# Optimization experiments

Hardware: AMD Instinct MI355X
Metric: run time of the kernel (lower is better)

The kernel has to match this reference:

```python
import jax, jax.numpy as jnp
import numpy as np

N_NODES = 100000
N_EDGES = 3200000
F_IN = 512
F_OUT = 256


def setup_inputs() -> dict:
    key = jax.random.key(0)
    k1, k2, k3, k4, k5 = jax.random.split(key, 5)
    x = jax.random.normal(k1, (N_NODES, F_IN), dtype=jnp.float32)
    weights = jax.random.normal(k2, (F_IN, F_OUT), dtype=jnp.float32) * 0.05
    # sparse adjacency in COO, row-sorted (equivalent to the CSR torch.spmm uses)
    edge_row = jnp.sort(jax.random.randint(k3, (N_EDGES,), 0, N_NODES, dtype=jnp.int32))
    edge_col = jax.random.randint(k4, (N_EDGES,), 0, N_NODES, dtype=jnp.int32)
    edge_val = jax.random.uniform(k5, (N_EDGES,), dtype=jnp.float32)
    return {"x": x, "weights": weights, "edge_row": edge_row,
            "edge_col": edge_col, "edge_val": edge_val}


def reference(x, weights, edge_row, edge_col, edge_val):
    # support = input @ weights  (dense GEMM)
    support = jnp.matmul(x, weights)                      # [N, F_OUT]
    # output = spmm(adj, support): gather neighbor rows, scale, scatter-add
    gathered = support[edge_col] * edge_val[:, None]      # [E, F_OUT]
    out = jax.ops.segment_sum(gathered, edge_row, num_segments=N_NODES)
    return out
```

## Files before the change

### kernel.cpp

```cpp
#include <hip/hip_runtime.h>

#define N_NODES 100000
#define N_EDGES 3200000
#define F_IN 512
#define F_OUT 256

typedef short bf16x8 __attribute__((ext_vector_type(8)));
typedef short bf16x4 __attribute__((ext_vector_type(4)));
typedef float f32x4 __attribute__((ext_vector_type(4)));
typedef unsigned u32x4 __attribute__((ext_vector_type(4)));

__device__ __forceinline__ short f2b(float f) {
    unsigned u = __builtin_bit_cast(unsigned, f);
    u += 0x7fffu + ((u >> 16) & 1u);
    return (short)(u >> 16);
}
__device__ __forceinline__ float b2f(short s) {
    unsigned u = ((unsigned)(unsigned short)s) << 16;
    return __builtin_bit_cast(float, u);
}
__device__ __forceinline__ unsigned pack2(float f0, float f1) {
    unsigned u0 = __builtin_bit_cast(unsigned, f0) + 0x8000u;
    unsigned u1 = __builtin_bit_cast(unsigned, f1) + 0x8000u;
    return __builtin_amdgcn_perm(u1, u0, 0x07060302);
}
__device__ __forceinline__ void load_lds16(const void* g, void* l) {
    __builtin_amdgcn_global_load_lds(
        (const __attribute__((address_space(1))) unsigned*)g,
        (__attribute__((address_space(3))) unsigned*)l, 16, 0, 0);
}

__global__ void k_wconv(const float* __restrict__ W, short* __restrict__ Wt) {
    int idx = blockIdx.x * 256 + threadIdx.x;
    int k = idx >> 8;
    int n = idx & 255;
    Wt[n * F_IN + k] = f2b(W[idx]);
}

__global__ void k_rowptr(const int* __restrict__ erow, int* __restrict__ rp) {
    int i = blockIdx.x * 256 + threadIdx.x;
    if (i > N_NODES) return;
    int lo = 0, hi = N_EDGES;
    while (lo < hi) {
        int mid = (lo + hi) >> 1;
        if (erow[mid] < i) lo = mid + 1; else hi = mid;
    }
    rp[i] = lo;
}

__global__ __launch_bounds__(512, 4) void k_gemm(const float* __restrict__ X,
                                                 const short* __restrict__ Wt,
                                                 short* __restrict__ S) {
    __shared__ char lds[65536];
    char* ldsA = lds;
    char* ldsB = lds + 32768;
    const int tid  = threadIdx.x;
    const int wave = tid >> 6;
    const int lane = tid & 63;
    const int wr   = wave >> 2;
    const int wc   = wave & 3;
    const int l15  = lane & 15, quad = lane >> 4;
    const long row_base = (long)blockIdx.x * 128;

    f32x4 acc[4][4];
#pragma unroll
    for (int i = 0; i < 4; ++i)
#pragma unroll
        for (int j = 0; j < 4; ++j) acc[i][j] = (f32x4){0.f, 0.f, 0.f, 0.f};

    const int srow = tid >> 3;
    const int schunk = (tid & 7) ^ (srow & 7);
    long gr0 = row_base + srow;
    long gr1 = gr0 + 64;
    if (gr0 >= N_NODES) gr0 = N_NODES - 1;
    if (gr1 >= N_NODES) gr1 = N_NODES - 1;
    const float* gp0 = X + gr0 * F_IN + schunk * 4;
    const float* gp1 = X + gr1 * F_IN + schunk * 4;

    const int bidx0 = wave * 128 + lane;
    const int bn0 = bidx0 >> 2, bs0 = bidx0 & 3;
    const int bidx1 = bidx0 + 64;
    const int bn1 = bidx1 >> 2, bs1 = bidx1 & 3;
    const short* bsrc0 = Wt + bn0 * F_IN + (bs0 ^ (bn0 & 3)) * 8;
    const short* bsrc1 = Wt + bn1 * F_IN + (bs1 ^ (bn1 & 3)) * 8;

    const int sw = l15 & 7;
    const int c0 = ((quad * 2) ^ sw) * 16;
    const int c1 = ((quad * 2 + 1) ^ sw) * 16;
    const int arow_byte = (wr * 64 + l15) * 128;
    const int bchunk = (quad ^ (l15 & 3)) * 16;
    const int brow_byte = (wc * 64 + l15) * 64;

    {
        char* a0 = ldsA + wave * 1024;
        load_lds16(gp0, a0);
        load_lds16(gp1, a0 + 8192);
        char* b0 = ldsB + wave * 2048;
        load_lds16(bsrc0, b0);
        load_lds16(bsrc1, b0 + 1024);
    }

#pragma unroll 1
    for (int k0 = 0; k0 < F_IN; k0 += 32) {
        const int cur = (k0 >> 5) & 1;
        if (k0 + 32 < F_IN) {
            const int kk = k0 + 32;
            char* a0 = ldsA + (cur ^ 1) * 16384 + wave * 1024;
            load_lds16(gp0 + kk, a0);
            load_lds16(gp1 + kk, a0 + 8192);
            char* b0 = ldsB + (cur ^ 1) * 16384 + wave * 2048;
            load_lds16(bsrc0 + kk, b0);
            load_lds16(bsrc1 + kk, b0 + 1024);
            asm volatile("s_waitcnt vmcnt(4)" ::: "memory");
        } else {
            asm volatile("s_waitcnt vmcnt(0)" ::: "memory");
        }
        __builtin_amdgcn_s_barrier();

        const char* abase = ldsA + cur * 16384 + arow_byte;
        const char* bbase = ldsB + cur * 16384 + brow_byte;
        bf16x8 bfrag[4];
#pragma unroll
        for (int j = 0; j < 4; ++j)
            bfrag[j] = *(const bf16x8*)(bbase + j * 1024 + bchunk);
#pragma unroll
        for (int i = 0; i < 4; ++i) {
            const char* ap = abase + i * 16 * 128;
            f32x4 x0 = *(const f32x4*)(ap + c0);
            f32x4 x1 = *(const f32x4*)(ap + c1);
            u32x4 pv = { pack2(x0.x, x0.y), pack2(x0.z, x0.w),
                         pack2(x1.x, x1.y), pack2(x1.z, x1.w) };
            bf16x8 afrag = __builtin_bit_cast(bf16x8, pv);
#pragma unroll
            for (int j = 0; j < 4; ++j)
                acc[i][j] = __builtin_amdgcn_mfma_f32_16x16x32_bf16(
                    afrag, bfrag[j], acc[i][j], 0, 0, 0);
        }

        asm volatile("s_waitcnt lgkmcnt(0)" ::: "memory");
        __builtin_amdgcn_s_barrier();
    }

#pragma unroll
    for (int i = 0; i < 4; ++i) {
#pragma unroll
        for (int rg = 0; rg < 4; ++rg) {
            long gm = row_base + wr * 64 + i * 16 + quad * 4 + rg;
            if (gm < N_NODES) {
#pragma unroll
                for (int j = 0; j < 4; ++j) {
                    int gn = wc * 64 + j * 16 + l15;
                    S[gm * F_OUT + gn] = f2b(acc[i][j][rg]);
                }
            }
        }
    }
}

__global__ __launch_bounds__(256) void k_spmm(const short* __restrict__ S,
                                              const int* __restrict__ ecol,
                                              const float* __restrict__ ev,
                                              const int* __restrict__ rp,
                                              float* __restrict__ out) {
    const int wid  = __builtin_amdgcn_readfirstlane((int)(threadIdx.x >> 6));
    const int lane = threadIdx.x & 63;
    const int r = blockIdx.x * 4 + wid;
    const int lo = __builtin_amdgcn_readfirstlane(rp[r]);
    const int hi = __builtin_amdgcn_readfirstlane(rp[r + 1]);
    const short* sp = S + lane * 4;
    float a0 = 0.f, a1 = 0.f, a2 = 0.f, a3 = 0.f;

#pragma unroll 1
    for (int base = lo; base < hi; base += 8) {
        int cc[8]; float vv[8];
#pragma unroll
        for (int u = 0; u < 8; ++u) {
            int e = base + u;
            int ee = e < hi ? e : hi - 1;
            cc[u] = __builtin_amdgcn_readfirstlane(ecol[ee]);
            int vb = __builtin_bit_cast(int, e < hi ? ev[ee] : 0.f);
            vv[u] = __builtin_bit_cast(float, __builtin_amdgcn_readfirstlane(vb));
        }
        bf16x4 g[8];
#pragma unroll
        for (int u = 0; u < 8; ++u)
            g[u] = *(const bf16x4*)(sp + cc[u] * 256);
#pragma unroll
        for (int u = 0; u < 8; ++u) {
            a0 += vv[u] * b2f(g[u][0]);
            a1 += vv[u] * b2f(g[u][1]);
            a2 += vv[u] * b2f(g[u][2]);
            a3 += vv[u] * b2f(g[u][3]);
        }
    }
    f32x4 o = {a0, a1, a2, a3};
    *(f32x4*)(out + (long)r * F_OUT + lane * 4) = o;
}

extern "C" void kernel_launch(void* const* d_in, const int* in_sizes, int n_in,
                              void* d_out, int out_size, void* d_ws, size_t ws_size,
                              hipStream_t stream) {
    const float* x    = (const float*)d_in[0];
    const float* w    = (const float*)d_in[1];
    const int*   erow = (const int*)d_in[2];
    const int*   ecol = (const int*)d_in[3];
    const float* ev   = (const float*)d_in[4];
    float* out = (float*)d_out;

    char* ws = (char*)d_ws;
    short* Wt = (short*)ws;
    int*   rp = (int*)(ws + 262144);
    short* S  = (short*)(ws + (1 << 20));

    k_wconv<<<512, 256, 0, stream>>>(w, Wt);
    k_rowptr<<<(N_NODES + 256) / 256, 256, 0, stream>>>(erow, rp);
    k_gemm<<<(N_NODES + 127) / 128, 512, 0, stream>>>(x, Wt, S);
    k_spmm<<<N_NODES / 4, 256, 0, stream>>>(S, ecol, ev, rp, out);
}
```

Baseline: 579.1 us.

## Merge prep kernels, retune B LDS swizzle, prefetch edge indices in SpMM

```diff
diff --git a/kernel.cpp b/kernel.cpp
--- a/kernel.cpp
+++ b/kernel.cpp
@@ -30,22 +30,24 @@
         (__attribute__((address_space(3))) unsigned*)l, 16, 0, 0);
 }
 
-__global__ void k_wconv(const float* __restrict__ W, short* __restrict__ Wt) {
-    int idx = blockIdx.x * 256 + threadIdx.x;
-    int k = idx >> 8;
-    int n = idx & 255;
-    Wt[n * F_IN + k] = f2b(W[idx]);
-}
-
-__global__ void k_rowptr(const int* __restrict__ erow, int* __restrict__ rp) {
-    int i = blockIdx.x * 256 + threadIdx.x;
-    if (i > N_NODES) return;
-    int lo = 0, hi = N_EDGES;
-    while (lo < hi) {
-        int mid = (lo + hi) >> 1;
-        if (erow[mid] < i) lo = mid + 1; else hi = mid;
-    }
-    rp[i] = lo;
+__global__ void k_prep(const float* __restrict__ W, short* __restrict__ Wt,
+                       const int* __restrict__ erow, int* __restrict__ rp) {
+    int b = blockIdx.x;
+    if (b < 512) {
+        int idx = b * 256 + threadIdx.x;
+        int k = idx >> 8;
+        int n = idx & 255;
+        Wt[n * F_IN + k] = f2b(W[idx]);
+    } else {
+        int i = (b - 512) * 256 + threadIdx.x;
+        if (i > N_NODES) return;
+        int lo = 0, hi = N_EDGES;
+        while (lo < hi) {
+            int mid = (lo + hi) >> 1;
+            if (erow[mid] < i) lo = mid + 1; else hi = mid;
+        }
+        rp[i] = lo;
+    }
 }
 
 __global__ __launch_bounds__(512, 4) void k_gemm(const float* __restrict__ X,
@@ -81,14 +83,14 @@
     const int bn0 = bidx0 >> 2, bs0 = bidx0 & 3;
     const int bidx1 = bidx0 + 64;
     const int bn1 = bidx1 >> 2, bs1 = bidx1 & 3;
-    const short* bsrc0 = Wt + bn0 * F_IN + (bs0 ^ (bn0 & 3)) * 8;
-    const short* bsrc1 = Wt + bn1 * F_IN + (bs1 ^ (bn1 & 3)) * 8;
+    const short* bsrc0 = Wt + bn0 * F_IN + (bs0 ^ ((bn0 >> 1) & 3)) * 8;
+    const short* bsrc1 = Wt + bn1 * F_IN + (bs1 ^ ((bn1 >> 1) & 3)) * 8;
 
     const int sw = l15 & 7;
     const int c0 = ((quad * 2) ^ sw) * 16;
     const int c1 = ((quad * 2 + 1) ^ sw) * 16;
     const int arow_byte = (wr * 64 + l15) * 128;
-    const int bchunk = (quad ^ (l15 & 3)) * 16;
+    const int bchunk = (quad ^ ((l15 >> 1) & 3)) * 16;
     const int brow_byte = (wc * 64 + l15) * 64;
 
     {
@@ -170,28 +172,45 @@
     const short* sp = S + lane * 4;
     float a0 = 0.f, a1 = 0.f, a2 = 0.f, a3 = 0.f;
 
-#pragma unroll 1
-    for (int base = lo; base < hi; base += 8) {
-        int cc[8]; float vv[8];
+    int cc[8]; float vv[8];
+    if (lo < hi) {
 #pragma unroll
         for (int u = 0; u < 8; ++u) {
-            int e = base + u;
+            int e = lo + u;
             int ee = e < hi ? e : hi - 1;
             cc[u] = __builtin_amdgcn_readfirstlane(ecol[ee]);
             int vb = __builtin_bit_cast(int, e < hi ? ev[ee] : 0.f);
             vv[u] = __builtin_bit_cast(float, __builtin_amdgcn_readfirstlane(vb));
         }
+    }
+#pragma unroll 1
+    for (int base = lo; base < hi; base += 8) {
         bf16x4 g[8];
 #pragma unroll
         for (int u = 0; u < 8; ++u)
             g[u] = *(const bf16x4*)(sp + cc[u] * 256);
+        int nb = base + 8;
+        int nc[8]; float nv[8];
+        if (nb < hi) {
+#pragma unroll
+            for (int u = 0; u < 8; ++u) {
+                int e = nb + u;
+                int ee = e < hi ? e : hi - 1;
+                nc[u] = __builtin_amdgcn_readfirstlane(ecol[ee]);
+                int vb = __builtin_bit_cast(int, e < hi ? ev[ee] : 0.f);
+                nv[u] = __builtin_bit_cast(float, __builtin_amdgcn_readfirstlane(vb));
+            }
+        }
 #pragma unroll
         for (int u = 0; u < 8; ++u) {
-            a0 += vv[u] * b2f(g[u][0]);
-            a1 += vv[u] * b2f(g[u][1]);
-            a2 += vv[u] * b2f(g[u][2]);
-            a3 += vv[u] * b2f(g[u][3]);
-        }
+            float v = vv[u];
+            a0 += v * b2f(g[u][0]);
+            a1 += v * b2f(g[u][1]);
+            a2 += v * b2f(g[u][2]);
+            a3 += v * b2f(g[u][3]);
+        }
+#pragma unroll
+        for (int u = 0; u < 8; ++u) { cc[u] = nc[u]; vv[u] = nv[u]; }
     }
     f32x4 o = {a0, a1, a2, a3};
     *(f32x4*)(out + (long)r * F_OUT + lane * 4) = o;
@@ -212,8 +231,7 @@
     int*   rp = (int*)(ws + 262144);
     short* S  = (short*)(ws + (1 << 20));
 
-    k_wconv<<<512, 256, 0, stream>>>(w, Wt);
-    k_rowptr<<<(N_NODES + 256) / 256, 256, 0, stream>>>(erow, rp);
+    k_prep<<<512 + (N_NODES + 256) / 256, 256, 0, stream>>>(w, Wt, erow, rp);
     k_gemm<<<(N_NODES + 127) / 128, 512, 0, stream>>>(x, Wt, S);
     k_spmm<<<N_NODES / 4, 256, 0, stream>>>(S, ecol, ev, rp, out);
 }
```

Measured after the change: 576.9 us. Within noise of the previous version (-0.4%).
